# Kernel optimization log

Measured on AMD Instinct MI355X. Metric: run time of the kernel, lower is better.

The kernel has to match this reference:

```python
import jax, jax.numpy as jnp
import numpy as np

BS, S1, S2, D_IN1, D_IN2, ATTN_DIM, HEADS = 4, 2048, 2048, 512, 512, 512, 8
HEAD_DIM = ATTN_DIM // HEADS
NEG = -1e23


def _layer_norm(x, g, b, eps=1e-5):
    m = jnp.mean(x, axis=-1, keepdims=True)
    v = jnp.mean((x - m) ** 2, axis=-1, keepdims=True)
    return (x - m) / jnp.sqrt(v + eps) * g + b


def setup_inputs() -> dict:
    key = jax.random.key(0)
    ks = jax.random.split(key, 12)
    s = 0.02
    return {
        "modal1": jax.random.normal(ks[0], (BS, S1, D_IN1), dtype=jnp.float32),
        "modal2": jax.random.normal(ks[1], (BS, S2, D_IN2), dtype=jnp.float32),
        "unpadding_mask1": jax.random.randint(ks[2], (BS, S1, 1), 0, 2, dtype=jnp.int32),
        "unpadding_mask2": jax.random.randint(ks[3], (BS, S2), 0, 2, dtype=jnp.int32),
        "Wq": jax.random.normal(ks[4], (D_IN1, ATTN_DIM), dtype=jnp.float32) * s,
        "bq": jnp.zeros((ATTN_DIM,), dtype=jnp.float32),
        "Wkv": jax.random.normal(ks[5], (D_IN2, ATTN_DIM), dtype=jnp.float32) * s,
        "bkv": jnp.zeros((ATTN_DIM,), dtype=jnp.float32),
        "ln1_g": jnp.ones((ATTN_DIM,), dtype=jnp.float32),
        "ln1_b": jnp.zeros((ATTN_DIM,), dtype=jnp.float32),
        "W1": jax.random.normal(ks[6], (ATTN_DIM, ATTN_DIM), dtype=jnp.float32) * s,
        "b1": jnp.zeros((ATTN_DIM,), dtype=jnp.float32),
        "W2": jax.random.normal(ks[7], (ATTN_DIM, ATTN_DIM), dtype=jnp.float32) * s,
        "b2": jnp.zeros((ATTN_DIM,), dtype=jnp.float32),
        "ln2_g": jnp.ones((ATTN_DIM,), dtype=jnp.float32),
        "ln2_b": jnp.zeros((ATTN_DIM,), dtype=jnp.float32),
    }


def reference(modal1, modal2, unpadding_mask1, unpadding_mask2,
              Wq, bq, Wkv, bkv, ln1_g, ln1_b, W1, b1, W2, b2, ln2_g, ln2_b):
    bs = modal1.shape[0]
    q = modal1 @ Wq + bq                       # (bs, s1, D)
    kv = modal2 @ Wkv + bkv                    # (bs, s2, D)
    q = q.reshape(bs, -1, HEADS, HEAD_DIM).transpose(0, 2, 1, 3)    # (bs,h,s1,hd)
    k = kv.reshape(bs, -1, HEADS, HEAD_DIM).transpose(0, 2, 1, 3)   # (bs,h,s2,hd)
    v = k                                       # original reuses k as v (no v_proj)
    # padding mask: (bs,s1,1) x (bs,1,s2) -> (bs,s1,s2) > 0
    m1 = unpadding_mask1.astype(jnp.float32)            # (bs, s1, 1)
    m2 = unpadding_mask2.astype(jnp.float32)[:, None, :]  # (bs, 1, s2)
    attn_mask = (m1 @ m2) > 0                            # (bs, s1, s2)
    scale = 1.0 / (float(ATTN_DIM) ** 0.5)               # NOTE: attn_dim, not head_dim
    logits = jnp.einsum('bhqd,bhkd->bhqk', q, k) * scale
    logits = logits + jnp.where(attn_mask[:, None, :, :], 0.0, NEG)
    attn = jax.nn.softmax(logits, axis=-1)
    attn_res = jnp.einsum('bhqk,bhkd->bhqd', attn, v)
    attn_res = attn_res.transpose(0, 2, 1, 3).reshape(bs, -1, ATTN_DIM)
    # dropout in eval mode == identity
    x = attn_res + modal1
    x = _layer_norm(x, ln1_g, ln1_b)
    residual = x
    _ffn_out = jnp.tanh(x @ W1 + b1) @ W2 + b2  # computed then DISCARDED (original bug)
    x = attn_res + residual                      # x = dropout(attn_res) + residual
    x = _layer_norm(x, ln2_g, ln2_b)
    return x
```

## Files before the change

kernel.cpp:

```cpp
#include <hip/hip_runtime.h>
#include <hip/hip_bf16.h>

#define BSZ 4
#define S1v 2048
#define S2v 2048
#define DM 512
#define NH 8
#define HD 64
#define SCALE 0.044194173824159216f
#define L2E 1.4426950408889634f
#define SC_L2E (0.044194173824159216f * 1.4426950408889634f)
#define CBIAS 0.0028152f
#define NEGB (-1e30f)

typedef __bf16 bf16x8 __attribute__((ext_vector_type(8)));
typedef float f32x4 __attribute__((ext_vector_type(4)));

__device__ __forceinline__ unsigned short f2bf(float f) {
  union { float f; unsigned u; } v; v.f = f;
  unsigned r = v.u + 0x7FFFu + ((v.u >> 16) & 1u);
  return (unsigned short)(r >> 16);
}
__device__ __forceinline__ unsigned asu(float f) {
  union { float f; unsigned u; } v; v.f = f; return v.u;
}

__global__ __launch_bounds__(256)
void wtrans(const float* __restrict__ W0, const float* __restrict__ W1,
            unsigned short* __restrict__ T0, unsigned short* __restrict__ T1) {
  __shared__ float tile[32][33];
  const float* W = blockIdx.z ? W1 : W0;
  unsigned short* Wt = blockIdx.z ? T1 : T0;
  const int tx = threadIdx.x, ty = threadIdx.y;
  const int n0 = blockIdx.x * 32, k0 = blockIdx.y * 32;
#pragma unroll
  for (int i = 0; i < 32; i += 8)
    tile[ty + i][tx] = W[(size_t)(k0 + ty + i) * DM + n0 + tx];
  __syncthreads();
#pragma unroll
  for (int i = 0; i < 32; i += 8)
    Wt[(size_t)(n0 + ty + i) * DM + k0 + tx] = f2bf(tile[tx][ty + i]);
}

__global__ __launch_bounds__(256)
void proj_gemm(const float* __restrict__ X0, const float* __restrict__ X1,
               const unsigned short* __restrict__ Wt0, const unsigned short* __restrict__ Wt1,
               const float* __restrict__ bias0, const float* __restrict__ bias1,
               unsigned short* __restrict__ Y0, unsigned short* __restrict__ Y1,
               unsigned short* __restrict__ Kt) {
  __shared__ unsigned short Xs[128][72];
  __shared__ unsigned short Ws[128][72];
  __shared__ unsigned short T2[128][136];
  const float* X = blockIdx.z ? X1 : X0;
  const unsigned short* Wt = blockIdx.z ? Wt1 : Wt0;
  const float* bias = blockIdx.z ? bias1 : bias0;
  unsigned short* Y = blockIdx.z ? Y1 : Y0;
  const int tid = threadIdx.x;
  const int wv = tid >> 6, lane = tid & 63;
  const int ln = lane & 15, qd = lane >> 4, q8 = qd * 8;
  const int wm = (wv >> 1) * 64, wn = (wv & 1) * 64;
  const int m0 = blockIdx.x * 128, n0 = blockIdx.y * 128;
  f32x4 acc[4][4] = {};
  for (int k0 = 0; k0 < DM; k0 += 64) {
    __syncthreads();
#pragma unroll
    for (int i = 0; i < 8; ++i) {
      int cid = tid + i * 256;
      int r = cid >> 4, c4 = (cid & 15) * 4;
      const float4 v = *(const float4*)(X + (size_t)(m0 + r) * DM + k0 + c4);
      ushort4 bv;
      bv.x = f2bf(v.x); bv.y = f2bf(v.y); bv.z = f2bf(v.z); bv.w = f2bf(v.w);
      *(ushort4*)&Xs[r][c4] = bv;
    }
#pragma unroll
    for (int i = 0; i < 4; ++i) {
      int cid = tid + i * 256;
      int r = cid >> 3, ch = (cid & 7) * 8;
      *(uint4*)&Ws[r][ch] = *(const uint4*)(Wt + (size_t)(n0 + r) * DM + k0 + ch);
    }
    __syncthreads();
#pragma unroll
    for (int kk = 0; kk < 2; ++kk) {
      bf16x8 aF[4], bF[4];
#pragma unroll
      for (int i = 0; i < 4; ++i)
        aF[i] = *(const bf16x8*)&Xs[wm + 16 * i + ln][kk * 32 + q8];
#pragma unroll
      for (int j = 0; j < 4; ++j)
        bF[j] = *(const bf16x8*)&Ws[wn + 16 * j + ln][kk * 32 + q8];
#pragma unroll
      for (int i = 0; i < 4; ++i)
#pragma unroll
        for (int j = 0; j < 4; ++j)
          acc[i][j] = __builtin_amdgcn_mfma_f32_16x16x32_bf16(aF[i], bF[j], acc[i][j], 0, 0, 0);
    }
  }
#pragma unroll
  for (int i = 0; i < 4; ++i)
#pragma unroll
    for (int j = 0; j < 4; ++j) {
      const int n = n0 + wn + 16 * j + ln;
      const float bb = bias[n];
#pragma unroll
      for (int r = 0; r < 4; ++r) {
        const int m = m0 + wm + 16 * i + qd * 4 + r;
        const unsigned short yb = f2bf(acc[i][j][r] + bb);
        Y[(size_t)m * DM + n] = yb;
        if (blockIdx.z) T2[wm + 16 * i + qd * 4 + r][wn + 16 * j + ln] = yb;
      }
    }
  if (blockIdx.z) {
    __syncthreads();
    const int b = m0 >> 11, s0 = m0 & 2047;
    const int h0 = n0 >> 6;
#pragma unroll
    for (int i = 0; i < 8; ++i) {
      const int cid = tid + i * 256;
      const int nl = cid >> 4, a = cid & 15;
      const int hh = h0 + (nl >> 6), d = nl & 63;
      const int base = 16 * (a >> 2) + 4 * (a & 3);
      ushort4 v0, v1;
      v0.x = T2[base + 0][nl]; v0.y = T2[base + 1][nl];
      v0.z = T2[base + 2][nl]; v0.w = T2[base + 3][nl];
      v1.x = T2[base + 64][nl]; v1.y = T2[base + 65][nl];
      v1.z = T2[base + 66][nl]; v1.w = T2[base + 67][nl];
      unsigned short* o =
          Kt + ((size_t)((b * 8 + hh) * HD + d)) * (size_t)S2v + s0 + a * 8;
      *(ushort4*)o = v0;
      *(ushort4*)(o + 4) = v1;
    }
  }
}

__global__ __launch_bounds__(256, 2)
void flash_attn(const unsigned short* __restrict__ Qb, const unsigned short* __restrict__ Kb,
                const unsigned short* __restrict__ Kt, const int* __restrict__ m1,
                const int* __restrict__ m2, float* __restrict__ attn) {
  __shared__ unsigned short Ks[2][128][72];
  __shared__ unsigned short Vts[2][64][136];
  __shared__ float m2f[2][128];

  const int tid = threadIdx.x;
  const int wv = tid >> 6, lane = tid & 63;
  const int ln = lane & 15, qd = lane >> 4, q8 = qd * 8;
  const int lin = blockIdx.x + (blockIdx.y << 4);
  const int lid = ((lin & 7) << 6) | (lin >> 3);
  const int bh = lid >> 4;
  const int b = bh >> 3, h = bh & 7;
  const int q0 = (lid & 15) << 7;

  const int rK = tid >> 3, cK = (tid & 7) * 8;
  const int rV = tid >> 4, cV = (tid & 15) * 8;
  const unsigned short* kbase = Kb + ((size_t)(b * S2v) + rK) * DM + h * HD + cK;
  const unsigned short* vbase = Kt + ((size_t)(bh * HD + rV)) * (size_t)S2v + cV;

  bf16x8 aQ[2][2];
#pragma unroll
  for (int t = 0; t < 2; ++t) {
    const size_t rbase =
        ((size_t)(b * S1v + q0 + wv * 32 + t * 16 + ln)) * DM + h * HD;
    aQ[t][0] = *(const bf16x8*)(Qb + rbase + q8);
    aQ[t][1] = *(const bf16x8*)(Qb + rbase + 32 + q8);
  }

  float acoef[2];
#pragma unroll
  for (int t = 0; t < 2; ++t)
    acoef[t] = (m1[b * S1v + q0 + wv * 32 + t * 16 + ln] == 0) ? 0.f : 1.f;

  float lrow[2] = {};
  f32x4 O[2][4] = {};

#pragma unroll
  for (int i = 0; i < 4; ++i)
    *(uint4*)&Ks[0][rK + i * 32][cK] = *(const uint4*)(kbase + (size_t)(i * 32) * DM);
#pragma unroll
  for (int i = 0; i < 4; ++i)
    *(uint4*)&Vts[0][rV + i * 16][cV] =
        *(const uint4*)(vbase + (size_t)(i * 16) * (size_t)S2v);
  if (tid < 128) m2f[0][tid] = (m2[b * S2v + tid] != 0) ? 0.f : NEGB;
  __syncthreads();

  for (int it = 0; it < 16; ++it) {
    const int cur = it & 1;
    const bool pf = (it != 15);

    uint4 nk[4], nv[4]; float nm = 0.f;
    if (pf) {
      const int sn = (it + 1) << 7;
#pragma unroll
      for (int i = 0; i < 4; ++i)
        nk[i] = *(const uint4*)(kbase + ((size_t)sn + (size_t)(i * 32)) * DM);
#pragma unroll
      for (int i = 0; i < 4; ++i)
        nv[i] = *(const uint4*)(vbase + sn + (size_t)(i * 16) * (size_t)S2v);
      if (tid < 128) nm = (m2[b * S2v + sn + tid] != 0) ? 0.f : NEGB;
    }

    f32x4 sc[2][8];
#pragma unroll
    for (int j = 0; j < 8; ++j) {
      const bf16x8 k0f = *(const bf16x8*)&Ks[cur][16 * j + ln][q8];
      const bf16x8 k1f = *(const bf16x8*)&Ks[cur][16 * j + ln][32 + q8];
#pragma unroll
      for (int t = 0; t < 2; ++t) {
        f32x4 z = {};
        z = __builtin_amdgcn_mfma_f32_16x16x32_bf16(k0f, aQ[t][0], z, 0, 0, 0);
        sc[t][j] = __builtin_amdgcn_mfma_f32_16x16x32_bf16(k1f, aQ[t][1], z, 0, 0, 0);
      }
    }

#pragma unroll
    for (int j = 0; j < 8; ++j) {
      const f32x4 mv = *(const f32x4*)&m2f[cur][16 * j + 4 * qd];
#pragma unroll
      for (int t = 0; t < 2; ++t)
#pragma unroll
        for (int r = 0; r < 4; ++r) {
          const float e = fmaf(acoef[t], fmaf(sc[t][j][r], SC_L2E, mv[r]), CBIAS);
          const float p = __builtin_amdgcn_exp2f(e);
          lrow[t] += p;
          sc[t][j][r] = p;
        }
    }

#pragma unroll
    for (int kk = 0; kk < 4; ++kk) {
      bf16x8 aP[2];
#pragma unroll
      for (int t = 0; t < 2; ++t) {
        union { uint4 u; bf16x8 v; } cvt;
        cvt.u.x = __builtin_amdgcn_perm(asu(sc[t][kk][1]),     asu(sc[t][kk][0]),     0x07060302u);
        cvt.u.y = __builtin_amdgcn_perm(asu(sc[t][kk][3]),     asu(sc[t][kk][2]),     0x07060302u);
        cvt.u.z = __builtin_amdgcn_perm(asu(sc[t][kk + 4][1]), asu(sc[t][kk + 4][0]), 0x07060302u);
        cvt.u.w = __builtin_amdgcn_perm(asu(sc[t][kk + 4][3]), asu(sc[t][kk + 4][2]), 0x07060302u);
        aP[t] = cvt.v;
      }
#pragma unroll
      for (int jn = 0; jn < 4; ++jn) {
        const bf16x8 bV = *(const bf16x8*)&Vts[cur][16 * jn + ln][kk * 32 + q8];
        O[0][jn] = __builtin_amdgcn_mfma_f32_16x16x32_bf16(aP[0], bV, O[0][jn], 0, 0, 0);
        O[1][jn] = __builtin_amdgcn_mfma_f32_16x16x32_bf16(aP[1], bV, O[1][jn], 0, 0, 0);
      }
    }

    if (pf) {
#pragma unroll
      for (int i = 0; i < 4; ++i) *(uint4*)&Ks[cur ^ 1][rK + i * 32][cK] = nk[i];
#pragma unroll
      for (int i = 0; i < 4; ++i) *(uint4*)&Vts[cur ^ 1][rV + i * 16][cV] = nv[i];
      if (tid < 128) m2f[cur ^ 1][tid] = nm;
      __syncthreads();
    }
  }

  float inv[2];
#pragma unroll
  for (int t = 0; t < 2; ++t) {
    float l = lrow[t];
    l += __shfl_xor(l, 16, 64);
    l += __shfl_xor(l, 32, 64);
    inv[t] = l > 0.f ? 1.0f / l : 0.f;
  }
#pragma unroll
  for (int t = 0; t < 2; ++t)
#pragma unroll
    for (int r = 0; r < 4; ++r) {
      const float invr = __shfl(inv[t], 4 * qd + r, 64);
      const int m = q0 + wv * 32 + t * 16 + qd * 4 + r;
#pragma unroll
      for (int jn = 0; jn < 4; ++jn)
        attn[((size_t)(b * S1v + m)) * DM + h * HD + 16 * jn + ln] = O[t][jn][r] * invr;
    }
}

__global__ __launch_bounds__(128)
void ln_fused(const float* __restrict__ attn, const float* __restrict__ modal1,
              const float* __restrict__ g1, const float* __restrict__ b1,
              const float* __restrict__ g2, const float* __restrict__ b2,
              float* __restrict__ out) {
  __shared__ float red[4];
  const int row = blockIdx.x, t = threadIdx.x;
  const size_t base = (size_t)row * DM + t * 4;
  const float4 a = *(const float4*)(attn + base);
  const float4 mo = *(const float4*)(modal1 + base);
  float av[4] = { a.x, a.y, a.z, a.w };
  float x[4] = { a.x + mo.x, a.y + mo.y, a.z + mo.z, a.w + mo.w };
  float s = 0.f, q = 0.f;
#pragma unroll
  for (int i = 0; i < 4; ++i) { s += x[i]; q += x[i] * x[i]; }
#pragma unroll
  for (int m = 1; m < 64; m <<= 1) { s += __shfl_xor(s, m, 64); q += __shfl_xor(q, m, 64); }
  if ((t & 63) == 0) { red[t >> 6] = s; red[2 + (t >> 6)] = q; }
  __syncthreads();
  s = red[0] + red[1]; q = red[2] + red[3];
  const float mu = s * (1.0f / DM);
  const float rinv = rsqrtf(q * (1.0f / DM) - mu * mu + 1e-5f);
  const int c = t * 4;
  const float4 G1 = *(const float4*)(g1 + c), B1 = *(const float4*)(b1 + c);
  const float gg1[4] = { G1.x, G1.y, G1.z, G1.w }, bb1[4] = { B1.x, B1.y, B1.z, B1.w };
  float y[4];
  float s2 = 0.f, q2 = 0.f;
#pragma unroll
  for (int i = 0; i < 4; ++i) {
    y[i] = av[i] + (x[i] - mu) * rinv * gg1[i] + bb1[i];
    s2 += y[i]; q2 += y[i] * y[i];
  }
#pragma unroll
  for (int m = 1; m < 64; m <<= 1) { s2 += __shfl_xor(s2, m, 64); q2 += __shfl_xor(q2, m, 64); }
  __syncthreads();
  if ((t & 63) == 0) { red[t >> 6] = s2; red[2 + (t >> 6)] = q2; }
  __syncthreads();
  s2 = red[0] + red[1]; q2 = red[2] + red[3];
  const float mu2 = s2 * (1.0f / DM);
  const float rinv2 = rsqrtf(q2 * (1.0f / DM) - mu2 * mu2 + 1e-5f);
  const float4 G2 = *(const float4*)(g2 + c), B2 = *(const float4*)(b2 + c);
  float4 o;
  o.x = (y[0] - mu2) * rinv2 * G2.x + B2.x;
  o.y = (y[1] - mu2) * rinv2 * G2.y + B2.y;
  o.z = (y[2] - mu2) * rinv2 * G2.z + B2.z;
  o.w = (y[3] - mu2) * rinv2 * G2.w + B2.w;
  *(float4*)(out + base) = o;
}

extern "C" void kernel_launch(void* const* d_in, const int* in_sizes, int n_in,
                              void* d_out, int out_size, void* d_ws, size_t ws_size,
                              hipStream_t stream) {
  const float* modal1 = (const float*)d_in[0];
  const float* modal2 = (const float*)d_in[1];
  const int*   m1     = (const int*)d_in[2];
  const int*   m2     = (const int*)d_in[3];
  const float* Wq     = (const float*)d_in[4];
  const float* bq     = (const float*)d_in[5];
  const float* Wkv    = (const float*)d_in[6];
  const float* bkv    = (const float*)d_in[7];
  const float* g1     = (const float*)d_in[8];
  const float* b1     = (const float*)d_in[9];
  const float* g2     = (const float*)d_in[14];
  const float* b2     = (const float*)d_in[15];
  float* out = (float*)d_out;

  char* ws = (char*)d_ws;
  unsigned short* q_bf  = (unsigned short*)(ws);
  unsigned short* k_bf  = (unsigned short*)(ws + 8388608);
  unsigned short* kt_bf = (unsigned short*)(ws + 16777216);
  unsigned short* wqt   = (unsigned short*)(ws + 25165824);
  unsigned short* wkt   = (unsigned short*)(ws + 25690112);
  float*          attn  = (float*)(ws + 26214400);

  dim3 tb(32, 8);
  wtrans<<<dim3(16, 16, 2), tb, 0, stream>>>(Wq, Wkv, wqt, wkt);
  proj_gemm<<<dim3(64, 4, 2), 256, 0, stream>>>(modal1, modal2, wqt, wkt,
                                                bq, bkv, q_bf, k_bf, kt_bf);
  flash_attn<<<dim3(16, 32), 256, 0, stream>>>(q_bf, k_bf, kt_bf, m1, m2, attn);
  ln_fused<<<dim3(8192), 128, 0, stream>>>(attn, modal1, g1, b1, g2, b2, out);
}
```

Baseline: 184.6 us.

## Load K/V MFMA fragments directly from global memory, dropping LDS staging

Removes the double-buffered LDS tiles for K and V and the per-iteration barrier. Each wave now loads its MFMA operand fragments straight from global memory (relying on L2/L1 for reuse across the four waves), and the whole key mask row is preloaded into LDS once. This cuts LDS traffic and synchronisation, but each wave now refetches the same K/V data, and the loads use narrower strided access with no software prefetch overlap.

New measurement: 253.0 us. 37.0% more time.

```diff
diff --git a/kernel.cpp b/kernel.cpp
--- a/kernel.cpp
+++ b/kernel.cpp
@@ -136,9 +136,7 @@
 void flash_attn(const unsigned short* __restrict__ Qb, const unsigned short* __restrict__ Kb,
                 const unsigned short* __restrict__ Kt, const int* __restrict__ m1,
                 const int* __restrict__ m2, float* __restrict__ attn) {
-  __shared__ unsigned short Ks[2][128][72];
-  __shared__ unsigned short Vts[2][64][136];
-  __shared__ float m2f[2][128];
+  __shared__ float m2f[2048];
 
   const int tid = threadIdx.x;
   const int wv = tid >> 6, lane = tid & 63;
@@ -149,10 +147,12 @@
   const int b = bh >> 3, h = bh & 7;
   const int q0 = (lid & 15) << 7;
 
-  const int rK = tid >> 3, cK = (tid & 7) * 8;
-  const int rV = tid >> 4, cV = (tid & 15) * 8;
-  const unsigned short* kbase = Kb + ((size_t)(b * S2v) + rK) * DM + h * HD + cK;
-  const unsigned short* vbase = Kt + ((size_t)(bh * HD + rV)) * (size_t)S2v + cV;
+#pragma unroll
+  for (int i = 0; i < 8; ++i)
+    m2f[tid + i * 256] = (m2[b * S2v + tid + i * 256] != 0) ? 0.f : NEGB;
+
+  const unsigned short* krow = Kb + ((size_t)(b * S2v) + ln) * DM + h * HD + q8;
+  const unsigned short* vrow = Kt + ((size_t)(bh * HD + ln)) * (size_t)S2v + q8;
 
   bf16x8 aQ[2][2];
 #pragma unroll
@@ -171,48 +171,32 @@
   float lrow[2] = {};
   f32x4 O[2][4] = {};
 
-#pragma unroll
-  for (int i = 0; i < 4; ++i)
-    *(uint4*)&Ks[0][rK + i * 32][cK] = *(const uint4*)(kbase + (size_t)(i * 32) * DM);
-#pragma unroll
-  for (int i = 0; i < 4; ++i)
-    *(uint4*)&Vts[0][rV + i * 16][cV] =
-        *(const uint4*)(vbase + (size_t)(i * 16) * (size_t)S2v);
-  if (tid < 128) m2f[0][tid] = (m2[b * S2v + tid] != 0) ? 0.f : NEGB;
   __syncthreads();
 
   for (int it = 0; it < 16; ++it) {
-    const int cur = it & 1;
-    const bool pf = (it != 15);
-
-    uint4 nk[4], nv[4]; float nm = 0.f;
-    if (pf) {
-      const int sn = (it + 1) << 7;
-#pragma unroll
-      for (int i = 0; i < 4; ++i)
-        nk[i] = *(const uint4*)(kbase + ((size_t)sn + (size_t)(i * 32)) * DM);
-#pragma unroll
-      for (int i = 0; i < 4; ++i)
-        nv[i] = *(const uint4*)(vbase + sn + (size_t)(i * 16) * (size_t)S2v);
-      if (tid < 128) nm = (m2[b * S2v + sn + tid] != 0) ? 0.f : NEGB;
+    const int s0 = it << 7;
+
+    bf16x8 kf[8][2];
+#pragma unroll
+    for (int j = 0; j < 8; ++j) {
+      const unsigned short* kr = krow + (size_t)(s0 + 16 * j) * DM;
+      kf[j][0] = *(const bf16x8*)(kr);
+      kf[j][1] = *(const bf16x8*)(kr + 32);
     }
 
     f32x4 sc[2][8];
 #pragma unroll
-    for (int j = 0; j < 8; ++j) {
-      const bf16x8 k0f = *(const bf16x8*)&Ks[cur][16 * j + ln][q8];
-      const bf16x8 k1f = *(const bf16x8*)&Ks[cur][16 * j + ln][32 + q8];
+    for (int j = 0; j < 8; ++j)
 #pragma unroll
       for (int t = 0; t < 2; ++t) {
         f32x4 z = {};
-        z = __builtin_amdgcn_mfma_f32_16x16x32_bf16(k0f, aQ[t][0], z, 0, 0, 0);
-        sc[t][j] = __builtin_amdgcn_mfma_f32_16x16x32_bf16(k1f, aQ[t][1], z, 0, 0, 0);
+        z = __builtin_amdgcn_mfma_f32_16x16x32_bf16(kf[j][0], aQ[t][0], z, 0, 0, 0);
+        sc[t][j] = __builtin_amdgcn_mfma_f32_16x16x32_bf16(kf[j][1], aQ[t][1], z, 0, 0, 0);
       }
-    }
 
 #pragma unroll
     for (int j = 0; j < 8; ++j) {
-      const f32x4 mv = *(const f32x4*)&m2f[cur][16 * j + 4 * qd];
+      const f32x4 mv = *(const f32x4*)&m2f[s0 + 16 * j + 4 * qd];
 #pragma unroll
       for (int t = 0; t < 2; ++t)
 #pragma unroll
@@ -226,6 +210,11 @@
 
 #pragma unroll
     for (int kk = 0; kk < 4; ++kk) {
+      bf16x8 vf[4];
+#pragma unroll
+      for (int jn = 0; jn < 4; ++jn)
+        vf[jn] = *(const bf16x8*)(vrow + (size_t)(16 * jn) * (size_t)S2v +
+                                  s0 + kk * 32);
       bf16x8 aP[2];
 #pragma unroll
       for (int t = 0; t < 2; ++t) {
@@ -238,19 +227,9 @@
       }
 #pragma unroll
       for (int jn = 0; jn < 4; ++jn) {
-        const bf16x8 bV = *(const bf16x8*)&Vts[cur][16 * jn + ln][kk * 32 + q8];
-        O[0][jn] = __builtin_amdgcn_mfma_f32_16x16x32_bf16(aP[0], bV, O[0][jn], 0, 0, 0);
-        O[1][jn] = __builtin_amdgcn_mfma_f32_16x16x32_bf16(aP[1], bV, O[1][jn], 0, 0, 0);
+        O[0][jn] = __builtin_amdgcn_mfma_f32_16x16x32_bf16(aP[0], vf[jn], O[0][jn], 0, 0, 0);
+        O[1][jn] = __builtin_amdgcn_mfma_f32_16x16x32_bf16(aP[1], vf[jn], O[1][jn], 0, 0, 0);
       }
-    }
-
-    if (pf) {
-#pragma unroll
-      for (int i = 0; i < 4; ++i) *(uint4*)&Ks[cur ^ 1][rK + i * 32][cK] = nk[i];
-#pragma unroll
-      for (int i = 0; i < 4; ++i) *(uint4*)&Vts[cur ^ 1][rV + i * 16][cV] = nv[i];
-      if (tid < 128) m2f[cur ^ 1][tid] = nm;
-      __syncthreads();
     }
   }
 
```
